# Performance work log

Measured on AMD Instinct MI355X. Metric: run time of the kernel, lower is better.

Reference implementation:

```python
import jax, jax.numpy as jnp
import numpy as np

NMS_MAX_OUTPUTS = 2000
CLS_SCORE_THRESH = 0.7
IOU_THRESH = 0.3
USE_SIDE_REFINE = False
B, N_ANCHORS, N_VALID, NUM_CLASSES = 4, 20000, 12000, 2


def setup_inputs() -> dict:
    key = jax.random.key(0)
    k = jax.random.split(key, 7)
    deltas = 0.5 * jax.random.normal(k[0], (B, N_ANCHORS, 2), jnp.float32)
    side_deltas = 0.5 * jax.random.normal(k[1], (B, N_ANCHORS, 1), jnp.float32)
    class_logits = 2.0 * jax.random.normal(k[2], (B, N_ANCHORS, NUM_CLASSES), jnp.float32)
    # CTPN-style anchors: fixed width 16, heights in [11, 280], on a ~1600px page
    cx = jax.random.uniform(k[3], (N_VALID,), jnp.float32, 8.0, 1592.0)
    cy = jax.random.uniform(k[4], (N_VALID,), jnp.float32, 0.0, 1600.0)
    h = jax.random.uniform(k[5], (N_VALID,), jnp.float32, 11.0, 280.0)
    valid_anchors = jnp.stack([cx - 8.0, cy - h * 0.5, cx + 8.0, cy + h * 0.5], axis=1)
    valid_indices = jnp.sort(
        jax.random.choice(k[6], N_ANCHORS, (N_VALID,), replace=False)
    ).astype(jnp.int32)
    return {
        "deltas": deltas,
        "side_deltas": side_deltas,
        "class_logits": class_logits,
        "valid_anchors": valid_anchors,
        "valid_indices": valid_indices,
    }


def apply_regress(deltas, side_deltas, anchors, use_side_refine):
    # deltas [B,V,2], side_deltas [B,V,1], anchors [V,4] -> [B,V,4]
    w = anchors[:, 2] - anchors[:, 0]
    h = anchors[:, 3] - anchors[:, 1]
    cx = (anchors[:, 0] + anchors[:, 2]) * 0.5
    cy = (anchors[:, 1] + anchors[:, 3]) * 0.5
    d = jnp.concatenate([deltas, side_deltas], axis=-1) * jnp.array([0.1, 0.2, 0.1], deltas.dtype)
    dy, dh, dx = d[..., 0], d[..., 1], d[..., 2]
    cy = cy + dy * h
    cx = cx + dx * w
    h = h * jnp.exp(dh)
    y1 = cy - h * 0.5
    y2 = cy + h * 0.5
    if use_side_refine:
        x1 = jnp.maximum(cx - w * 0.5, 0.0)
        x2 = cx + w * 0.5
    else:
        x1 = jnp.broadcast_to(anchors[:, 0], y1.shape)
        x2 = jnp.broadcast_to(anchors[:, 2], y1.shape)
    return jnp.stack([x1, y1, x2, y2], axis=-1)


def nms_single(boxes, scores, logits, max_out, iou_t, score_t):
    """Greedy NMS (tf.image.non_max_suppression semantics) + gather + pad_to_fixed_size."""
    V = boxes.shape[0]
    order = jnp.argsort(-jax.lax.stop_gradient(scores))
    b, s, l = boxes[order], scores[order], logits[order]
    bc = jax.lax.stop_gradient(b)  # suppression decisions are non-differentiable
    x1, y1, x2, y2 = bc[:, 0], bc[:, 1], bc[:, 2], bc[:, 3]
    areas = (x2 - x1) * (y2 - y1)
    idxs = jnp.arange(V)
    valid = jax.lax.stop_gradient(s) > score_t

    def body(i, keep):
        xx1 = jnp.maximum(x1[i], x1)
        yy1 = jnp.maximum(y1[i], y1)
        xx2 = jnp.minimum(x2[i], x2)
        yy2 = jnp.minimum(y2[i], y2)
        inter = jnp.maximum(xx2 - xx1, 0.0) * jnp.maximum(yy2 - yy1, 0.0)
        iou = inter / (areas[i] + areas - inter + 1e-10)
        sup = (iou > iou_t) & (idxs > i)
        return jnp.where(keep[i], keep & ~sup, keep)

    keep = jax.lax.fori_loop(0, V, body, valid)
    rank = jnp.cumsum(keep.astype(jnp.int32)) - 1
    sel = keep & (rank < max_out)
    dest = jnp.where(sel, rank, max_out)  # overflow rows parked at row max_out, sliced off
    tag = jnp.ones((V, 1), b.dtype)

    def pad_fixed(x):
        # append tag column of 1s for real rows, scatter to fixed size, zero-pad rest
        aug = jnp.where(sel[:, None], jnp.concatenate([x, tag], axis=1), 0.0)
        out = jnp.zeros((max_out + 1, aug.shape[1]), aug.dtype).at[dest].set(aug)
        return out[:max_out]

    return pad_fixed(b), pad_fixed(s[:, None]), pad_fixed(l)


def reference(deltas, side_deltas, class_logits, valid_anchors, valid_indices):
    d = jnp.take(deltas, valid_indices, axis=1)
    sd = jnp.take(side_deltas, valid_indices, axis=1)
    cl = jnp.take(class_logits, valid_indices, axis=1)
    class_scores = jax.nn.softmax(cl, axis=-1)
    fg_scores = jnp.max(class_scores[..., 1:], axis=-1)  # [B,V]
    proposals = apply_regress(d, sd, valid_anchors, USE_SIDE_REFINE)  # [B,V,4]
    f = lambda bb, ss, ll: nms_single(bb, ss, ll, NMS_MAX_OUTPUTS, IOU_THRESH, CLS_SCORE_THRESH)
    boxes, box_scores, out_logits = jax.vmap(f)(proposals, fg_scores, cl)
    return boxes, box_scores, out_logits
```

## Files before the change

### kernel.cpp

```cpp
#include <hip/hip_runtime.h>
#include <cstdint>
#include <cstddef>

typedef unsigned long long u64;
typedef unsigned int u32;
typedef u32 u32x4 __attribute__((ext_vector_type(4)));

#define AS1 __attribute__((address_space(1)))
#define AS3 __attribute__((address_space(3)))

constexpr int kB = 4;
constexpr int kNA = 20000;
constexpr int kV = 12000;
constexpr int kCAP = 5120;
constexpr int kW = kCAP / 64;
constexpr int kIC = 256;
constexpr int kMAXOUT = 2000;
constexpr int kGPB = 40;
constexpr float kIOU = 0.3f;
constexpr float kSCORE = 0.7f;

static __device__ __forceinline__ u64 greedy64(u64 freeS, u32 d_lo, u32 d_hi) {
  u64 keptS;
  asm volatile(
      "s_mov_b64 s[40:41], %[free]\n\t"
      "s_mov_b64 s[42:43], 0\n\t"
      "GRD_%=:\n\t"
      "s_ff1_i32_b64 s44, s[40:41]\n\t"
      "s_cmp_eq_i32 s44, -1\n\t"
      "s_cbranch_scc1 GRDEND_%=\n\t"
      "s_bitset1_b64 s[42:43], s44\n\t"
      "s_bitset0_b64 s[40:41], s44\n\t"
      "v_readlane_b32 s46, %[dlo], s44\n\t"
      "v_readlane_b32 s47, %[dhi], s44\n\t"
      "s_nop 4\n\t"
      "s_andn2_b64 s[40:41], s[40:41], s[46:47]\n\t"
      "s_branch GRD_%=\n\t"
      "GRDEND_%=:\n\t"
      "s_mov_b64 %[kept], s[42:43]\n\t"
      : [kept] "=&s"(keptS)
      : [free] "s"(freeS), [dlo] "v"(d_lo), [dhi] "v"(d_hi)
      : "s40", "s41", "s42", "s43", "s44", "s45", "s46", "s47", "scc");
  return keptS;
}

__device__ __forceinline__ u64 waveOr64(u64 v) {
  v |= __shfl_xor((unsigned long long)v, 32, 64);
  v |= __shfl_xor((unsigned long long)v, 16, 64);
  v |= __shfl_xor((unsigned long long)v, 8, 64);
  v |= __shfl_xor((unsigned long long)v, 4, 64);
  v |= __shfl_xor((unsigned long long)v, 2, 64);
  v |= __shfl_xor((unsigned long long)v, 1, 64);
  return v;
}

__device__ __forceinline__ u64 readlane64u(u64 v, int l) {
  u32 lo = __builtin_amdgcn_readlane((u32)v, (u32)l);
  u32 hi = __builtin_amdgcn_readlane((u32)(v >> 32), (u32)l);
  return ((u64)hi << 32) | lo;
}

__global__ __launch_bounds__(256) void stage_score(
    const float* __restrict__ deltas, const float* __restrict__ logits,
    const float* __restrict__ anchors, const int* __restrict__ vidx,
    u32* __restrict__ counts, u64* __restrict__ keys,
    float* __restrict__ rec_y1, float* __restrict__ rec_y2,
    float* __restrict__ rec_l0, float* __restrict__ rec_l1) {
  int t = blockIdx.x * 256 + threadIdx.x;
  if (t >= kB * kV) return;
  int b = t / kV, i = t - b * kV;
  int lane = threadIdx.x & 63;
  int idx = vidx[i];
  float2 lg = *(const float2*)(logits + ((size_t)b * kNA + idx) * 2);
  float score = 1.0f / (1.0f + expf(lg.x - lg.y));
  if (!(score > kSCORE)) return;
  float2 dd = *(const float2*)(deltas + ((size_t)b * kNA + idx) * 2);
  float4 a = *(const float4*)(anchors + (size_t)i * 4);
  float h = a.w - a.y;
  float cy = (a.y + a.w) * 0.5f + (dd.x * 0.1f) * h;
  float hn = h * expf(dd.y * 0.2f);
  rec_y1[t] = cy - hn * 0.5f;
  rec_y2[t] = cy + hn * 0.5f;
  rec_l0[t] = lg.x;
  rec_l1[t] = lg.y;
  u64 act = __ballot(1);
  int b0 = (int)__builtin_amdgcn_readfirstlane((u32)b);
  u64 sameb = __ballot(b == b0);
  u64 grp = (b == b0) ? sameb : (act & ~sameb);
  u32 cnt = (u32)__popcll(grp);
  int lead = (int)__ffsll((unsigned long long)grp) - 1;
  u32 base = 0;
  if (lane == lead) base = atomicAdd(&counts[b], cnt);
  base = (u32)__shfl((int)base, lead, 64);
  u32 pos = base + (u32)__popcll(grp & ((1ULL << lane) - 1ULL));
  if (pos < kCAP) {
    u64 key = ((u64)(0xFFFFFFFFu - __float_as_uint(score)) << 32) | (u32)i;
    keys[(size_t)b * kCAP + pos] = key;
  }
}

__global__ __launch_bounds__(256) void rank_sort_emit(
    const u32* __restrict__ counts, const u64* __restrict__ keys,
    const float* __restrict__ rec_y1, const float* __restrict__ rec_y2,
    const float* __restrict__ rec_l0, const float* __restrict__ rec_l1,
    const float* __restrict__ anchors,
    float4* __restrict__ sbox, float* __restrict__ sarea,
    float* __restrict__ ssc, float* __restrict__ sl0, float* __restrict__ sl1) {
  __shared__ u64 sk[kCAP];
  int b = blockIdx.x / (kCAP / 256);
  int chunk = blockIdx.x % (kCAP / 256);
  int tid = threadIdx.x;
  int cnt = (int)min(counts[b], (u32)kCAP);
  for (int e = tid; e < kCAP; e += 256)
    sk[e] = (e < cnt) ? keys[(size_t)b * kCAP + e] : ~0ULL;
  __syncthreads();
  int s = chunk * 256 + tid;
  if (s >= cnt) return;
  u64 ks = sk[s];
  int rank = 0;
  for (int j = 0; j < kCAP; j += 8) {
#pragma unroll
    for (int u = 0; u < 8; ++u) rank += (sk[j + u] < ks) ? 1 : 0;
  }
  int i = (int)(u32)ks;
  float sc = __uint_as_float(0xFFFFFFFFu - (u32)(ks >> 32));
  float x1 = anchors[(size_t)i * 4 + 0], x2 = anchors[(size_t)i * 4 + 2];
  float y1 = rec_y1[b * kV + i], y2 = rec_y2[b * kV + i];
  size_t o = (size_t)b * kCAP + rank;
  sbox[o] = make_float4(x1, y1, x2, y2);
  sarea[o] = (x2 - x1) * (y2 - y1);
  ssc[o] = sc;
  sl0[o] = rec_l0[b * kV + i];
  sl1[o] = rec_l1[b * kV + i];
}

__global__ __launch_bounds__(256) void stage_mask(
    const u32* __restrict__ counts,
    const float4* __restrict__ sbox, const float* __restrict__ sarea,
    u64* __restrict__ mask) {
  __shared__ float4 sb[4][kIC];
  __shared__ float sa[4][kIC];
  int lane = threadIdx.x & 63;
  int wv = threadIdx.x >> 6;
  int gw = blockIdx.x * 4 + wv;
  int bt = gw & 3;
  int rest = gw >> 2;
  int jb = rest % kW;
  int ic = rest / kW;
  int M = (int)min(counts[bt], (u32)kCAP);
  int W = (M + 63) >> 6;
  if (jb >= W) return;
  int ibeg = ic * kIC;
  int iend = min(min(M, jb * 64 + 64), ibeg + kIC);
  if (ibeg >= iend) return;
  const float4* pb = sbox + (size_t)bt * kCAP;
  const float* pa = sarea + (size_t)bt * kCAP;
  u64* mb = mask + (size_t)bt * ((size_t)kW * kCAP);
#pragma unroll
  for (int r = 0; r < kIC / 64; ++r) {
    int e = r * 64 + lane;
    sb[wv][e] = pb[ibeg + e];
    sa[wv][e] = pa[ibeg + e];
  }
  int j = jb * 64 + lane;
  bool jv = (j < M);
  float4 bj = make_float4(0.f, 0.f, 0.f, 0.f);
  float aj = 0.f;
  if (jv) { bj = pb[j]; aj = pa[j]; }
#pragma unroll 4
  for (int i = ibeg; i < iend; ++i) {
    float4 bi = sb[wv][i - ibeg];
    float ai = sa[wv][i - ibeg];
    float xx1 = fmaxf(bi.x, bj.x);
    float yy1 = fmaxf(bi.y, bj.y);
    float xx2 = fminf(bi.z, bj.z);
    float yy2 = fminf(bi.w, bj.w);
    float inter = fmaxf(xx2 - xx1, 0.0f) * fmaxf(yy2 - yy1, 0.0f);
    float iou = inter / (ai + aj - inter + 1e-10f);
    bool sup = jv && (j > i) && (iou > kIOU);
    u64 wm = __ballot(sup);
    if (lane == 0)
      mb[(((size_t)(i >> 6)) * kW + jb) * 64 + (i & 63)] = wm;
  }
}

__global__ __launch_bounds__(64, 1) void stage_scan(
    const u32* __restrict__ counts, const u64* __restrict__ mask,
    u64* __restrict__ pub, int* __restrict__ keepidx, u32* __restrict__ kcnt) {
  __shared__ __align__(16) u64 col[80 * 128];
  const int bid = blockIdx.x;
  const int bt = bid & 3;
  const int g = bid >> 2;
  const int lane = threadIdx.x;
  const int M = (int)min(counts[bt], (u32)kCAP);
  const int W = (M + 63) >> 6;
  const int blk0 = 2 * g, blk1 = 2 * g + 1;
  if (blk0 >= W) return;
  const u64* mb = mask + (size_t)bt * ((size_t)kW * kCAP);
  u64* pp = pub + (size_t)(bt * kGPB) * 4;

  const int nstage = (blk1 < 79 ? blk1 : 79) + 1;
  for (int b = 0; b < nstage; ++b)
    __builtin_amdgcn_global_load_lds(
        (const AS1 u32*)(mb + ((size_t)b * kW + blk0) * 64 + (size_t)lane * 2),
        (AS3 u32*)&col[b * 128], 16, 0, 0);
  __builtin_amdgcn_s_waitcnt(0x0070);

  u64 acc0 = 0, acc1 = 0;
  u32 cum = 0;
  const u64* qa = pp + (size_t)lane * 2;
  const u64* qb = pp + 128 + (size_t)(lane & 15) * 2;
  int next = 0;
  while (next < g) {
    u32x4 ra, rb;
    asm volatile(
        "global_load_dwordx4 %0, %2, off sc0 sc1\n\t"
        "global_load_dwordx4 %1, %3, off sc0 sc1\n\t"
        "s_waitcnt vmcnt(0)"
        : "=&v"(ra), "=&v"(rb)
        : "v"(qa), "v"(qb)
        : "memory");
    u64 wA0 = ((u64)ra[1] << 32) | ra[0];
    u64 wA1 = ((u64)ra[3] << 32) | ra[2];
    u64 wB0 = ((u64)rb[1] << 32) | rb[0];
    u64 wB1 = ((u64)rb[3] << 32) | rb[2];
    u64 okA = __ballot(((wA0 & wA1) >> 63) != 0);
    u64 okB = __ballot(((wB0 & wB1) >> 63) != 0);
    int w = next;
    for (; w < g; ++w) {
      u64 km0, km1;
      if (w < 32) {
        if (((okA >> (2 * w)) & 3ULL) != 3ULL) break;
        km0 = (u64)(u32)readlane64u(wA0, 2 * w) |
              ((u64)(u32)readlane64u(wA1, 2 * w) << 32);
        km1 = (u64)(u32)readlane64u(wA0, 2 * w + 1) |
              ((u64)(u32)readlane64u(wA1, 2 * w + 1) << 32);
      } else {
        int l = 2 * (w - 32);
        if (((okB >> l) & 3ULL) != 3ULL) break;
        km0 = (u64)(u32)readlane64u(wB0, l) |
              ((u64)(u32)readlane64u(wB1, l) << 32);
        km1 = (u64)(u32)readlane64u(wB0, l + 1) |
              ((u64)(u32)readlane64u(wB1, l + 1) << 32);
      }
      cum += (u32)__popcll(km0) + (u32)__popcll(km1);
      if (km0 | km1) {
        bool k0 = (km0 >> lane) & 1ULL, k1 = (km1 >> lane) & 1ULL;
        u64 v = (k0 ? col[(2 * w) * 128 + lane] : 0ULL) |
                (k1 ? col[(2 * w + 1) * 128 + lane] : 0ULL);
        u64 u = (k0 ? col[(2 * w) * 128 + 64 + lane] : 0ULL) |
                (k1 ? col[(2 * w + 1) * 128 + 64 + lane] : 0ULL);
        acc0 |= waveOr64(v);
        acc1 |= waveOr64(u);
      }
    }
    next = w;
    if (next < g) __builtin_amdgcn_s_sleep(16);
  }

  u64 keptm0 = 0;
  const u32 cum0 = cum;
  if ((int)cum0 < kMAXOUT) {
    int remn = M - blk0 * 64;
    u64 validm = (remn >= 64) ? ~0ULL : ((1ULL << remn) - 1ULL);
    u64 freeb = ~acc0 & validm;
    u32 flo = __builtin_amdgcn_readfirstlane((u32)freeb);
    u32 fhi = __builtin_amdgcn_readfirstlane((u32)(freeb >> 32));
    u64 diag = col[blk0 * 128 + lane];
    keptm0 = greedy64(((u64)fhi << 32) | flo, (u32)diag, (u32)(diag >> 32));
  }
  cum = cum0 + (u32)__popcll(keptm0);
  if (keptm0) {
    u64 x = ((keptm0 >> lane) & 1ULL) ? col[blk0 * 128 + 64 + lane] : 0ULL;
    acc1 |= waveOr64(x);
  }
  u64 keptm1 = 0;
  const u32 cum1 = cum;
  if (blk1 < W && (int)cum1 < kMAXOUT) {
    int remn = M - blk1 * 64;
    u64 validm = (remn >= 64) ? ~0ULL : ((1ULL << remn) - 1ULL);
    u64 freeb = ~acc1 & validm;
    u32 flo = __builtin_amdgcn_readfirstlane((u32)freeb);
    u32 fhi = __builtin_amdgcn_readfirstlane((u32)(freeb >> 32));
    u64 diag = col[blk1 * 128 + 64 + lane];
    keptm1 = greedy64(((u64)fhi << 32) | flo, (u32)diag, (u32)(diag >> 32));
  }
  cum = cum1 + (u32)__popcll(keptm1);

  if (lane == 0) {
    const u64 F = 1ULL << 63;
    (void)__hip_atomic_fetch_or(&pp[(size_t)g * 4 + 0], F | (u64)(u32)keptm0,
                                __ATOMIC_RELAXED, __HIP_MEMORY_SCOPE_AGENT);
    (void)__hip_atomic_fetch_or(&pp[(size_t)g * 4 + 1], F | (u64)(u32)(keptm0 >> 32),
                                __ATOMIC_RELAXED, __HIP_MEMORY_SCOPE_AGENT);
    (void)__hip_atomic_fetch_or(&pp[(size_t)g * 4 + 2], F | (u64)(u32)keptm1,
                                __ATOMIC_RELAXED, __HIP_MEMORY_SCOPE_AGENT);
    (void)__hip_atomic_fetch_or(&pp[(size_t)g * 4 + 3], F | (u64)(u32)(keptm1 >> 32),
                                __ATOMIC_RELAXED, __HIP_MEMORY_SCOPE_AGENT);
  }
  if ((keptm0 >> lane) & 1ULL) {
    int rank = (int)cum0 + (int)__popcll(keptm0 & ((1ULL << lane) - 1ULL));
    if (rank < kMAXOUT) keepidx[bt * kMAXOUT + rank] = blk0 * 64 + lane;
  }
  if ((keptm1 >> lane) & 1ULL) {
    int rank = (int)cum1 + (int)__popcll(keptm1 & ((1ULL << lane) - 1ULL));
    if (rank < kMAXOUT) keepidx[bt * kMAXOUT + rank] = blk1 * 64 + lane;
  }
  if (lane == 0 && g == (W - 1) / 2) kcnt[bt] = min(cum, (u32)kMAXOUT);
}

__global__ __launch_bounds__(256) void stage_out(
    const u32* __restrict__ kcnt, const int* __restrict__ keepidx,
    const float4* __restrict__ sbox, const float* __restrict__ ssc,
    const float* __restrict__ sl0, const float* __restrict__ sl1,
    float* __restrict__ out) {
  int t = blockIdx.x * 256 + threadIdx.x;
  if (t >= kB * kMAXOUT) return;
  int b = t / kMAXOUT, r = t - b * kMAXOUT;
  if (r >= (int)kcnt[b]) return;
  int i = keepidx[t];
  size_t o = (size_t)b * kCAP + i;
  float4 bx = sbox[o];
  float* boxes = out;
  float* bscores = out + (size_t)kB * kMAXOUT * 5;
  float* blogits = out + (size_t)kB * kMAXOUT * 7;
  boxes[(size_t)t * 5 + 0] = bx.x;
  boxes[(size_t)t * 5 + 1] = bx.y;
  boxes[(size_t)t * 5 + 2] = bx.z;
  boxes[(size_t)t * 5 + 3] = bx.w;
  boxes[(size_t)t * 5 + 4] = 1.0f;
  bscores[(size_t)t * 2 + 0] = ssc[o];
  bscores[(size_t)t * 2 + 1] = 1.0f;
  blogits[(size_t)t * 3 + 0] = sl0[o];
  blogits[(size_t)t * 3 + 1] = sl1[o];
  blogits[(size_t)t * 3 + 2] = 1.0f;
}

extern "C" void kernel_launch(void* const* d_in, const int* in_sizes, int n_in,
                              void* d_out, int out_size, void* d_ws, size_t ws_size,
                              hipStream_t stream) {
  const float* deltas = (const float*)d_in[0];
  const float* logits = (const float*)d_in[2];
  const float* anchors = (const float*)d_in[3];
  const int* vidx = (const int*)d_in[4];
  float* out = (float*)d_out;

  char* p = (char*)d_ws;
  auto take = [&](size_t bytes) -> char* {
    char* r = p;
    p += (bytes + 255) & ~(size_t)255;
    return r;
  };
  u32* counts = (u32*)take(kB * sizeof(u32));
  u32* kcnt = (u32*)take(kB * sizeof(u32));
  u64* pub = (u64*)take((size_t)kB * kGPB * 4 * sizeof(u64));
  u64* keys = (u64*)take((size_t)kB * kCAP * sizeof(u64));
  float* rec_y1 = (float*)take((size_t)kB * kV * sizeof(float));
  float* rec_y2 = (float*)take((size_t)kB * kV * sizeof(float));
  float* rec_l0 = (float*)take((size_t)kB * kV * sizeof(float));
  float* rec_l1 = (float*)take((size_t)kB * kV * sizeof(float));
  float4* sbox = (float4*)take((size_t)kB * kCAP * sizeof(float4));
  float* sarea = (float*)take((size_t)kB * kCAP * sizeof(float));
  float* ssc = (float*)take((size_t)kB * kCAP * sizeof(float));
  float* sl0 = (float*)take((size_t)kB * kCAP * sizeof(float));
  float* sl1 = (float*)take((size_t)kB * kCAP * sizeof(float));
  int* keepidx = (int*)take((size_t)kB * kMAXOUT * sizeof(int));
  u64* mask = (u64*)take((size_t)kB * kCAP * kW * sizeof(u64) + 4096);

  (void)hipMemsetAsync(out, 0, (size_t)out_size * sizeof(float), stream);
  (void)hipMemsetAsync(counts, 0, 5632, stream);

  stage_score<<<(kB * kV + 255) / 256, 256, 0, stream>>>(
      deltas, logits, anchors, vidx, counts, keys, rec_y1, rec_y2, rec_l0, rec_l1);
  rank_sort_emit<<<kB * (kCAP / 256), 256, 0, stream>>>(
      counts, keys, rec_y1, rec_y2, rec_l0, rec_l1, anchors,
      sbox, sarea, ssc, sl0, sl1);
  stage_mask<<<kB * kW * (kCAP / kIC) / 4, 256, 0, stream>>>(
      counts, sbox, sarea, mask);
  stage_scan<<<kB * kGPB, 64, 0, stream>>>(counts, mask, pub, keepidx, kcnt);
  stage_out<<<(kB * kMAXOUT + 255) / 256, 256, 0, stream>>>(
      kcnt, keepidx, sbox, ssc, sl0, sl1, out);
}
```

Before: 361.3 us.

## Fuse rank-sort, IoU mask and scan into one kernel with flag handoff

Merges the rank-sort emit, IoU mask build and greedy scan kernels into one launch. Rank blocks signal completion per batch through an atomic counter. Scan blocks spin on that counter and then compute their own 128-column slab of the suppression mask directly into LDS, so the global mask buffer and two kernel launches disappear. In exchange, each scan block recomputes IoU over all preceding rows with only one wave, so mask work is far less parallel than before. The spin-wait also relies on the rank blocks being scheduled alongside or ahead of the scan blocks.

```diff
diff --git a/kernel.cpp b/kernel.cpp
--- a/kernel.cpp
+++ b/kernel.cpp
@@ -14,9 +14,9 @@
 constexpr int kV = 12000;
 constexpr int kCAP = 5120;
 constexpr int kW = kCAP / 64;
-constexpr int kIC = 256;
 constexpr int kMAXOUT = 2000;
 constexpr int kGPB = 40;
+constexpr int kRWG = kCAP / 256;
 constexpr float kIOU = 0.3f;
 constexpr float kSCORE = 0.7f;
 
@@ -99,112 +99,110 @@
   }
 }
 
-__global__ __launch_bounds__(256) void rank_sort_emit(
+__global__ __launch_bounds__(256, 1) void fused_rank_scan(
     const u32* __restrict__ counts, const u64* __restrict__ keys,
     const float* __restrict__ rec_y1, const float* __restrict__ rec_y2,
     const float* __restrict__ rec_l0, const float* __restrict__ rec_l1,
     const float* __restrict__ anchors,
     float4* __restrict__ sbox, float* __restrict__ sarea,
-    float* __restrict__ ssc, float* __restrict__ sl0, float* __restrict__ sl1) {
-  __shared__ u64 sk[kCAP];
-  int b = blockIdx.x / (kCAP / 256);
-  int chunk = blockIdx.x % (kCAP / 256);
-  int tid = threadIdx.x;
-  int cnt = (int)min(counts[b], (u32)kCAP);
-  for (int e = tid; e < kCAP; e += 256)
-    sk[e] = (e < cnt) ? keys[(size_t)b * kCAP + e] : ~0ULL;
-  __syncthreads();
-  int s = chunk * 256 + tid;
-  if (s >= cnt) return;
-  u64 ks = sk[s];
-  int rank = 0;
-  for (int j = 0; j < kCAP; j += 8) {
+    float* __restrict__ ssc, float* __restrict__ sl0, float* __restrict__ sl1,
+    u32* __restrict__ rankdone, u64* __restrict__ pub,
+    int* __restrict__ keepidx, u32* __restrict__ kcnt) {
+  __shared__ __align__(16) char smem[87040];
+  const int bid = blockIdx.x;
+
+  if (bid < kB * kRWG) {
+    u64* sk = (u64*)smem;
+    int b = bid / kRWG;
+    int chunk = bid % kRWG;
+    int tid = threadIdx.x;
+    int cnt = (int)min(counts[b], (u32)kCAP);
+    for (int e = tid; e < kCAP; e += 256)
+      sk[e] = (e < cnt) ? keys[(size_t)b * kCAP + e] : ~0ULL;
+    __syncthreads();
+    int s = chunk * 256 + tid;
+    if (s < cnt) {
+      u64 ks = sk[s];
+      int rank = 0;
+      for (int j = 0; j < kCAP; j += 8) {
 #pragma unroll
-    for (int u = 0; u < 8; ++u) rank += (sk[j + u] < ks) ? 1 : 0;
-  }
-  int i = (int)(u32)ks;
-  float sc = __uint_as_float(0xFFFFFFFFu - (u32)(ks >> 32));
-  float x1 = anchors[(size_t)i * 4 + 0], x2 = anchors[(size_t)i * 4 + 2];
-  float y1 = rec_y1[b * kV + i], y2 = rec_y2[b * kV + i];
-  size_t o = (size_t)b * kCAP + rank;
-  sbox[o] = make_float4(x1, y1, x2, y2);
-  sarea[o] = (x2 - x1) * (y2 - y1);
-  ssc[o] = sc;
-  sl0[o] = rec_l0[b * kV + i];
-  sl1[o] = rec_l1[b * kV + i];
-}
-
-__global__ __launch_bounds__(256) void stage_mask(
-    const u32* __restrict__ counts,
-    const float4* __restrict__ sbox, const float* __restrict__ sarea,
-    u64* __restrict__ mask) {
-  __shared__ float4 sb[4][kIC];
-  __shared__ float sa[4][kIC];
-  int lane = threadIdx.x & 63;
-  int wv = threadIdx.x >> 6;
-  int gw = blockIdx.x * 4 + wv;
-  int bt = gw & 3;
-  int rest = gw >> 2;
-  int jb = rest % kW;
-  int ic = rest / kW;
-  int M = (int)min(counts[bt], (u32)kCAP);
-  int W = (M + 63) >> 6;
-  if (jb >= W) return;
-  int ibeg = ic * kIC;
-  int iend = min(min(M, jb * 64 + 64), ibeg + kIC);
-  if (ibeg >= iend) return;
-  const float4* pb = sbox + (size_t)bt * kCAP;
-  const float* pa = sarea + (size_t)bt * kCAP;
-  u64* mb = mask + (size_t)bt * ((size_t)kW * kCAP);
-#pragma unroll
-  for (int r = 0; r < kIC / 64; ++r) {
-    int e = r * 64 + lane;
-    sb[wv][e] = pb[ibeg + e];
-    sa[wv][e] = pa[ibeg + e];
-  }
-  int j = jb * 64 + lane;
-  bool jv = (j < M);
-  float4 bj = make_float4(0.f, 0.f, 0.f, 0.f);
-  float aj = 0.f;
-  if (jv) { bj = pb[j]; aj = pa[j]; }
-#pragma unroll 4
-  for (int i = ibeg; i < iend; ++i) {
-    float4 bi = sb[wv][i - ibeg];
-    float ai = sa[wv][i - ibeg];
-    float xx1 = fmaxf(bi.x, bj.x);
-    float yy1 = fmaxf(bi.y, bj.y);
-    float xx2 = fminf(bi.z, bj.z);
-    float yy2 = fminf(bi.w, bj.w);
-    float inter = fmaxf(xx2 - xx1, 0.0f) * fmaxf(yy2 - yy1, 0.0f);
-    float iou = inter / (ai + aj - inter + 1e-10f);
-    bool sup = jv && (j > i) && (iou > kIOU);
-    u64 wm = __ballot(sup);
-    if (lane == 0)
-      mb[(((size_t)(i >> 6)) * kW + jb) * 64 + (i & 63)] = wm;
-  }
-}
-
-__global__ __launch_bounds__(64, 1) void stage_scan(
-    const u32* __restrict__ counts, const u64* __restrict__ mask,
-    u64* __restrict__ pub, int* __restrict__ keepidx, u32* __restrict__ kcnt) {
-  __shared__ __align__(16) u64 col[80 * 128];
-  const int bid = blockIdx.x;
-  const int bt = bid & 3;
-  const int g = bid >> 2;
+        for (int u = 0; u < 8; ++u) rank += (sk[j + u] < ks) ? 1 : 0;
+      }
+      int i = (int)(u32)ks;
+      float sc = __uint_as_float(0xFFFFFFFFu - (u32)(ks >> 32));
+      float x1 = anchors[(size_t)i * 4 + 0], x2 = anchors[(size_t)i * 4 + 2];
+      float y1 = rec_y1[b * kV + i], y2 = rec_y2[b * kV + i];
+      size_t o = (size_t)b * kCAP + rank;
+      sbox[o] = make_float4(x1, y1, x2, y2);
+      sarea[o] = (x2 - x1) * (y2 - y1);
+      ssc[o] = sc;
+      sl0[o] = rec_l0[b * kV + i];
+      sl1[o] = rec_l1[b * kV + i];
+    }
+    __syncthreads();
+    if (threadIdx.x == 0)
+      (void)__hip_atomic_fetch_add(&rankdone[b], 1u, __ATOMIC_RELEASE,
+                                   __HIP_MEMORY_SCOPE_AGENT);
+    return;
+  }
+
+  if (threadIdx.x >= 64) return;
+  u64* col = (u64*)smem;
+  float4* icb = (float4*)(smem + 81920);
+  float* ica = (float*)(smem + 81920 + 4096);
+  const int sbid = bid - kB * kRWG;
+  const int bt = sbid & 3;
+  const int g = sbid >> 2;
   const int lane = threadIdx.x;
   const int M = (int)min(counts[bt], (u32)kCAP);
   const int W = (M + 63) >> 6;
   const int blk0 = 2 * g, blk1 = 2 * g + 1;
   if (blk0 >= W) return;
-  const u64* mb = mask + (size_t)bt * ((size_t)kW * kCAP);
   u64* pp = pub + (size_t)(bt * kGPB) * 4;
 
-  const int nstage = (blk1 < 79 ? blk1 : 79) + 1;
-  for (int b = 0; b < nstage; ++b)
-    __builtin_amdgcn_global_load_lds(
-        (const AS1 u32*)(mb + ((size_t)b * kW + blk0) * 64 + (size_t)lane * 2),
-        (AS3 u32*)&col[b * 128], 16, 0, 0);
-  __builtin_amdgcn_s_waitcnt(0x0070);
+  while (__hip_atomic_load(&rankdone[bt], __ATOMIC_ACQUIRE,
+                           __HIP_MEMORY_SCOPE_AGENT) < (u32)kRWG)
+    __builtin_amdgcn_s_sleep(32);
+
+  const float4* pb = sbox + (size_t)bt * kCAP;
+  const float* pa = sarea + (size_t)bt * kCAP;
+  const int j1 = g * 128 + lane, j2 = j1 + 64;
+  const bool jv1 = j1 < M, jv2 = j2 < M;
+  float4 bx1 = make_float4(0.f, 0.f, 0.f, 0.f), bx2 = bx1;
+  float aj1 = 0.f, aj2 = 0.f;
+  if (jv1) { bx1 = pb[j1]; aj1 = pa[j1]; }
+  if (jv2) { bx2 = pb[j2]; aj2 = pa[j2]; }
+
+  const int iMax = min(M, (blk1 + 1) * 64);
+  for (int ibeg = 0; ibeg < iMax; ibeg += 256) {
+#pragma unroll
+    for (int r2 = 0; r2 < 4; ++r2) {
+      int e = r2 * 64 + lane;
+      icb[e] = pb[ibeg + e];
+      ica[e] = pa[ibeg + e];
+    }
+    int iend = min(iMax, ibeg + 256);
+    for (int i = ibeg; i < iend; ++i) {
+      float4 bi = icb[i - ibeg];
+      float ai = ica[i - ibeg];
+      float xx1 = fmaxf(bi.x, bx1.x), yy1 = fmaxf(bi.y, bx1.y);
+      float xx2 = fminf(bi.z, bx1.z), yy2 = fminf(bi.w, bx1.w);
+      float in1 = fmaxf(xx2 - xx1, 0.0f) * fmaxf(yy2 - yy1, 0.0f);
+      float io1 = in1 / (ai + aj1 - in1 + 1e-10f);
+      bool s1 = jv1 && (j1 > i) && (io1 > kIOU);
+      float ux1 = fmaxf(bi.x, bx2.x), vy1 = fmaxf(bi.y, bx2.y);
+      float ux2 = fminf(bi.z, bx2.z), vy2 = fminf(bi.w, bx2.w);
+      float in2 = fmaxf(ux2 - ux1, 0.0f) * fmaxf(vy2 - vy1, 0.0f);
+      float io2 = in2 / (ai + aj2 - in2 + 1e-10f);
+      bool s2 = jv2 && (j2 > i) && (io2 > kIOU);
+      u64 w0 = __ballot(s1);
+      u64 w1 = __ballot(s2);
+      if (lane == 0) {
+        col[(i >> 6) * 128 + (i & 63)] = w0;
+        col[(i >> 6) * 128 + 64 + (i & 63)] = w1;
+      }
+    }
+  }
 
   u64 acc0 = 0, acc1 = 0;
   u32 cum = 0;
@@ -354,6 +352,7 @@
   u32* counts = (u32*)take(kB * sizeof(u32));
   u32* kcnt = (u32*)take(kB * sizeof(u32));
   u64* pub = (u64*)take((size_t)kB * kGPB * 4 * sizeof(u64));
+  u32* rankdone = (u32*)take(kB * sizeof(u32));
   u64* keys = (u64*)take((size_t)kB * kCAP * sizeof(u64));
   float* rec_y1 = (float*)take((size_t)kB * kV * sizeof(float));
   float* rec_y2 = (float*)take((size_t)kB * kV * sizeof(float));
@@ -365,19 +364,15 @@
   float* sl0 = (float*)take((size_t)kB * kCAP * sizeof(float));
   float* sl1 = (float*)take((size_t)kB * kCAP * sizeof(float));
   int* keepidx = (int*)take((size_t)kB * kMAXOUT * sizeof(int));
-  u64* mask = (u64*)take((size_t)kB * kCAP * kW * sizeof(u64) + 4096);
 
   (void)hipMemsetAsync(out, 0, (size_t)out_size * sizeof(float), stream);
-  (void)hipMemsetAsync(counts, 0, 5632, stream);
+  (void)hipMemsetAsync(counts, 0, 5888, stream);
 
   stage_score<<<(kB * kV + 255) / 256, 256, 0, stream>>>(
       deltas, logits, anchors, vidx, counts, keys, rec_y1, rec_y2, rec_l0, rec_l1);
-  rank_sort_emit<<<kB * (kCAP / 256), 256, 0, stream>>>(
+  fused_rank_scan<<<kB * kRWG + kB * kGPB, 256, 0, stream>>>(
       counts, keys, rec_y1, rec_y2, rec_l0, rec_l1, anchors,
-      sbox, sarea, ssc, sl0, sl1);
-  stage_mask<<<kB * kW * (kCAP / kIC) / 4, 256, 0, stream>>>(
-      counts, sbox, sarea, mask);
-  stage_scan<<<kB * kGPB, 64, 0, stream>>>(counts, mask, pub, keepidx, kcnt);
+      sbox, sarea, ssc, sl0, sl1, rankdone, pub, keepidx, kcnt);
   stage_out<<<(kB * kMAXOUT + 255) / 256, 256, 0, stream>>>(
       kcnt, keepidx, sbox, ssc, sl0, sl1, out);
 }
```

New measurement: 1.112 ms. 208% more time.

## Fuse output emission into NMS scan and coalesce suppression-mask stores

Applied to the files above, without the earlier changes.

The output gather kernel is removed and the scan kernel now writes boxes, scores and logits for each kept index directly, which drops one launch and the keepidx/kcnt round trip. In the mask kernel, each lane keeps the ballot word whose row matches its lane index, so each 64-row chunk is written with one coalesced store instead of 64 single-lane stores. The spin sleep in the scan wait loop is also shortened. The trade-off is that the output writes now sit on the serial scan's critical tail, and the memset size is adjusted to the smaller workspace.

```diff
diff --git a/kernel.cpp b/kernel.cpp
--- a/kernel.cpp
+++ b/kernel.cpp
@@ -167,26 +167,35 @@
   float4 bj = make_float4(0.f, 0.f, 0.f, 0.f);
   float aj = 0.f;
   if (jv) { bj = pb[j]; aj = pa[j]; }
+  for (int b0 = ibeg; b0 < iend; b0 += 64) {
+    int lim = min(iend - b0, 64);
+    u64 mywm = 0;
 #pragma unroll 4
-  for (int i = ibeg; i < iend; ++i) {
-    float4 bi = sb[wv][i - ibeg];
-    float ai = sa[wv][i - ibeg];
-    float xx1 = fmaxf(bi.x, bj.x);
-    float yy1 = fmaxf(bi.y, bj.y);
-    float xx2 = fminf(bi.z, bj.z);
-    float yy2 = fminf(bi.w, bj.w);
-    float inter = fmaxf(xx2 - xx1, 0.0f) * fmaxf(yy2 - yy1, 0.0f);
-    float iou = inter / (ai + aj - inter + 1e-10f);
-    bool sup = jv && (j > i) && (iou > kIOU);
-    u64 wm = __ballot(sup);
-    if (lane == 0)
-      mb[(((size_t)(i >> 6)) * kW + jb) * 64 + (i & 63)] = wm;
+    for (int k = 0; k < lim; ++k) {
+      int e = b0 - ibeg + k;
+      float4 bi = sb[wv][e];
+      float ai = sa[wv][e];
+      float xx1 = fmaxf(bi.x, bj.x);
+      float yy1 = fmaxf(bi.y, bj.y);
+      float xx2 = fminf(bi.z, bj.z);
+      float yy2 = fminf(bi.w, bj.w);
+      float inter = fmaxf(xx2 - xx1, 0.0f) * fmaxf(yy2 - yy1, 0.0f);
+      float iou = inter / (ai + aj - inter + 1e-10f);
+      bool sup = jv && (j > b0 + k) && (iou > kIOU);
+      u64 wm = __ballot(sup);
+      if (k == lane) mywm = wm;
+    }
+    if (lane < lim)
+      mb[(((size_t)(b0 >> 6)) * kW + jb) * 64 + lane] = mywm;
   }
 }
 
 __global__ __launch_bounds__(64, 1) void stage_scan(
     const u32* __restrict__ counts, const u64* __restrict__ mask,
-    u64* __restrict__ pub, int* __restrict__ keepidx, u32* __restrict__ kcnt) {
+    u64* __restrict__ pub,
+    const float4* __restrict__ sbox, const float* __restrict__ ssc,
+    const float* __restrict__ sl0, const float* __restrict__ sl1,
+    float* __restrict__ out) {
   __shared__ __align__(16) u64 col[80 * 128];
   const int bid = blockIdx.x;
   const int bt = bid & 3;
@@ -255,7 +264,7 @@
       }
     }
     next = w;
-    if (next < g) __builtin_amdgcn_s_sleep(16);
+    if (next < g) __builtin_amdgcn_s_sleep(8);
   }
 
   u64 keptm0 = 0;
@@ -298,42 +307,33 @@
     (void)__hip_atomic_fetch_or(&pp[(size_t)g * 4 + 3], F | (u64)(u32)(keptm1 >> 32),
                                 __ATOMIC_RELAXED, __HIP_MEMORY_SCOPE_AGENT);
   }
-  if ((keptm0 >> lane) & 1ULL) {
-    int rank = (int)cum0 + (int)__popcll(keptm0 & ((1ULL << lane) - 1ULL));
-    if (rank < kMAXOUT) keepidx[bt * kMAXOUT + rank] = blk0 * 64 + lane;
-  }
-  if ((keptm1 >> lane) & 1ULL) {
-    int rank = (int)cum1 + (int)__popcll(keptm1 & ((1ULL << lane) - 1ULL));
-    if (rank < kMAXOUT) keepidx[bt * kMAXOUT + rank] = blk1 * 64 + lane;
-  }
-  if (lane == 0 && g == (W - 1) / 2) kcnt[bt] = min(cum, (u32)kMAXOUT);
-}
-
-__global__ __launch_bounds__(256) void stage_out(
-    const u32* __restrict__ kcnt, const int* __restrict__ keepidx,
-    const float4* __restrict__ sbox, const float* __restrict__ ssc,
-    const float* __restrict__ sl0, const float* __restrict__ sl1,
-    float* __restrict__ out) {
-  int t = blockIdx.x * 256 + threadIdx.x;
-  if (t >= kB * kMAXOUT) return;
-  int b = t / kMAXOUT, r = t - b * kMAXOUT;
-  if (r >= (int)kcnt[b]) return;
-  int i = keepidx[t];
-  size_t o = (size_t)b * kCAP + i;
-  float4 bx = sbox[o];
+
   float* boxes = out;
   float* bscores = out + (size_t)kB * kMAXOUT * 5;
   float* blogits = out + (size_t)kB * kMAXOUT * 7;
-  boxes[(size_t)t * 5 + 0] = bx.x;
-  boxes[(size_t)t * 5 + 1] = bx.y;
-  boxes[(size_t)t * 5 + 2] = bx.z;
-  boxes[(size_t)t * 5 + 3] = bx.w;
-  boxes[(size_t)t * 5 + 4] = 1.0f;
-  bscores[(size_t)t * 2 + 0] = ssc[o];
-  bscores[(size_t)t * 2 + 1] = 1.0f;
-  blogits[(size_t)t * 3 + 0] = sl0[o];
-  blogits[(size_t)t * 3 + 1] = sl1[o];
-  blogits[(size_t)t * 3 + 2] = 1.0f;
+  auto emit = [&](int i, int rank) {
+    size_t o = (size_t)bt * kCAP + i;
+    float4 bx = sbox[o];
+    size_t t = (size_t)bt * kMAXOUT + rank;
+    boxes[t * 5 + 0] = bx.x;
+    boxes[t * 5 + 1] = bx.y;
+    boxes[t * 5 + 2] = bx.z;
+    boxes[t * 5 + 3] = bx.w;
+    boxes[t * 5 + 4] = 1.0f;
+    bscores[t * 2 + 0] = ssc[o];
+    bscores[t * 2 + 1] = 1.0f;
+    blogits[t * 3 + 0] = sl0[o];
+    blogits[t * 3 + 1] = sl1[o];
+    blogits[t * 3 + 2] = 1.0f;
+  };
+  if ((keptm0 >> lane) & 1ULL) {
+    int rank = (int)cum0 + (int)__popcll(keptm0 & ((1ULL << lane) - 1ULL));
+    if (rank < kMAXOUT) emit(blk0 * 64 + lane, rank);
+  }
+  if ((keptm1 >> lane) & 1ULL) {
+    int rank = (int)cum1 + (int)__popcll(keptm1 & ((1ULL << lane) - 1ULL));
+    if (rank < kMAXOUT) emit(blk1 * 64 + lane, rank);
+  }
 }
 
 extern "C" void kernel_launch(void* const* d_in, const int* in_sizes, int n_in,
@@ -352,7 +352,6 @@
     return r;
   };
   u32* counts = (u32*)take(kB * sizeof(u32));
-  u32* kcnt = (u32*)take(kB * sizeof(u32));
   u64* pub = (u64*)take((size_t)kB * kGPB * 4 * sizeof(u64));
   u64* keys = (u64*)take((size_t)kB * kCAP * sizeof(u64));
   float* rec_y1 = (float*)take((size_t)kB * kV * sizeof(float));
@@ -364,11 +363,10 @@
   float* ssc = (float*)take((size_t)kB * kCAP * sizeof(float));
   float* sl0 = (float*)take((size_t)kB * kCAP * sizeof(float));
   float* sl1 = (float*)take((size_t)kB * kCAP * sizeof(float));
-  int* keepidx = (int*)take((size_t)kB * kMAXOUT * sizeof(int));
   u64* mask = (u64*)take((size_t)kB * kCAP * kW * sizeof(u64) + 4096);
 
   (void)hipMemsetAsync(out, 0, (size_t)out_size * sizeof(float), stream);
-  (void)hipMemsetAsync(counts, 0, 5632, stream);
+  (void)hipMemsetAsync(counts, 0, 5376, stream);
 
   stage_score<<<(kB * kV + 255) / 256, 256, 0, stream>>>(
       deltas, logits, anchors, vidx, counts, keys, rec_y1, rec_y2, rec_l0, rec_l1);
@@ -377,7 +375,6 @@
       sbox, sarea, ssc, sl0, sl1);
   stage_mask<<<kB * kW * (kCAP / kIC) / 4, 256, 0, stream>>>(
       counts, sbox, sarea, mask);
-  stage_scan<<<kB * kGPB, 64, 0, stream>>>(counts, mask, pub, keepidx, kcnt);
-  stage_out<<<(kB * kMAXOUT + 255) / 256, 256, 0, stream>>>(
-      kcnt, keepidx, sbox, ssc, sl0, sl1, out);
-}
+  stage_scan<<<kB * kGPB, 64, 0, stream>>>(
+      counts, mask, pub, sbox, ssc, sl0, sl1, out);
+}
```

Measured after the change: 347.1 us. 3.9% less time.
